# Performance work log

Hardware: AMD Instinct MI355X
Metric: run time of the kernel (lower is better)

## Reference

```python
import jax, jax.numpy as jnp
import numpy as np

B, IN, OUT = 256, 1024, 1024

def leaky_clamp(x, lo, hi, slope):
    return jnp.where(x < lo, lo + slope * (x - lo),
           jnp.where(x > hi, hi + slope * (x - hi), x))

def setup_inputs() -> dict:
    key = jax.random.key(0)
    kx, kw = jax.random.split(key)
    x = jax.random.normal(kx, (B, IN), dtype=jnp.float32)
    # xavier_normal for (out,in): std = sqrt(2/(in+out))
    std = np.sqrt(2.0 / (IN + OUT)).astype(np.float32)
    weight = jax.random.normal(kw, (OUT, IN), dtype=jnp.float32) * std
    log_tau = jnp.zeros((), dtype=jnp.float32)
    return {"x": x, "weight": weight, "log_tau": log_tau}

def reference(x, weight, log_tau):
    # actual_weight = leaky_clamp(weight, 0, 1, 0.1)
    aw = leaky_clamp(weight, 0.0, 1.0, 0.1)          # (OUT, IN)
    tau = jnp.exp(log_tau)                            # scalar
    z = x[:, None, :] * aw[None, :, :]                # (B, OUT, IN)
    p = jax.nn.softmax(tau * z, axis=-1)              # (B, OUT, IN)
    s = jnp.sum(p * z, axis=-1)                       # (B, OUT)
    return s
```

## Files before the change

### kernel.cpp

```cpp
#include <hip/hip_runtime.h>

#define BB   256
#define IN_  1024
#define OUTN 1024

#define TB  16
#define TO  16
#define KC  256
#define NS  (IN_ / KC)
#define PAD 4

#define LOG2E 1.4426950408889634f

typedef float v2f __attribute__((ext_vector_type(2)));
typedef float v4f __attribute__((ext_vector_type(4)));

__device__ __forceinline__ float leaky_clamp01(float v) {
    return __builtin_amdgcn_fmed3f(v, 0.1f * v, fmaf(0.1f, v, 0.9f));
}

__global__ __launch_bounds__(256, 4)
void esm_fused_kernel(const float* __restrict__ x,
                      const float* __restrict__ w,
                      const float* __restrict__ log_tau,
                      float* __restrict__ out) {
    __shared__ float xs[TB][KC + PAD];
    __shared__ float wls[TO][KC + PAD];

    const int tid = threadIdx.x;
    const int bid = blockIdx.x;
    const int bt = bid >> 6;
    const int ot = bid & 63;
    const int b0 = bt * TB;
    const int o0 = ot * TO;

    const float scale = __expf(log_tau[0]) * LOG2E;

    const int h    = tid >> 6;
    const int cell = tid & 63;
    const int tx   = cell & 7;
    const int ty   = cell >> 3;
    const int ih   = h << 2;

    const int srow = tid >> 6;
    const int si4  = (tid & 63) << 2;

    float4 rx[4], rw[4];
    #pragma unroll
    for (int t = 0; t < 4; ++t) {
        const int row = srow + t * 4;
        rx[t] = *(const float4*)&x[(size_t)(b0 + row) * IN_ + si4];
        rw[t] = *(const float4*)&w[(size_t)(o0 + row) * IN_ + si4];
    }

    v2f d00 = {0.f, 0.f}, d01 = {0.f, 0.f}, d10 = {0.f, 0.f}, d11 = {0.f, 0.f};
    v2f n00 = {0.f, 0.f}, n01 = {0.f, 0.f}, n10 = {0.f, 0.f}, n11 = {0.f, 0.f};

    #pragma unroll
    for (int s = 0; s < NS; ++s) {
        if (s) __syncthreads();
        #pragma unroll
        for (int t = 0; t < 4; ++t) {
            const int row = srow + t * 4;
            const float4 xv = rx[t];
            float4 xo;
            xo.x = xv.x * scale; xo.y = xv.y * scale;
            xo.z = xv.z * scale; xo.w = xv.w * scale;
            *(float4*)&xs[row][si4] = xo;
            const float4 wv = rw[t];
            float4 wo;
            wo.x = leaky_clamp01(wv.x); wo.y = leaky_clamp01(wv.y);
            wo.z = leaky_clamp01(wv.z); wo.w = leaky_clamp01(wv.w);
            *(float4*)&wls[row][si4] = wo;
        }
        __syncthreads();
        if (s + 1 < NS) {
            const int i0n = (s + 1) * KC;
            #pragma unroll
            for (int t = 0; t < 4; ++t) {
                const int row = srow + t * 4;
                rx[t] = *(const float4*)&x[(size_t)(b0 + row) * IN_ + i0n + si4];
                rw[t] = *(const float4*)&w[(size_t)(o0 + row) * IN_ + i0n + si4];
            }
        }

        #pragma unroll 4
        for (int m = 0; m < KC / 16; ++m) {
            const int ib = 16 * m + ih;
            const v4f xa0 = *(const v4f*)&xs[2 * ty][ib];
            const v4f xa1 = *(const v4f*)&xs[2 * ty + 1][ib];
            const v4f wa0 = *(const v4f*)&wls[2 * tx][ib];
            const v4f wa1 = *(const v4f*)&wls[2 * tx + 1][ib];
            #pragma unroll
            for (int p = 0; p < 2; ++p) {
                const v2f xv0 = {xa0[2 * p], xa0[2 * p + 1]};
                const v2f xv1 = {xa1[2 * p], xa1[2 * p + 1]};
                const v2f wv0 = {wa0[2 * p], wa0[2 * p + 1]};
                const v2f wv1 = {wa1[2 * p], wa1[2 * p + 1]};
                const v2f t00 = xv0 * wv0;
                const v2f t01 = xv0 * wv1;
                const v2f t10 = xv1 * wv0;
                const v2f t11 = xv1 * wv1;
                v2f e00, e01, e10, e11;
                e00.x = __builtin_amdgcn_exp2f(t00.x);
                e00.y = __builtin_amdgcn_exp2f(t00.y);
                e01.x = __builtin_amdgcn_exp2f(t01.x);
                e01.y = __builtin_amdgcn_exp2f(t01.y);
                e10.x = __builtin_amdgcn_exp2f(t10.x);
                e10.y = __builtin_amdgcn_exp2f(t10.y);
                e11.x = __builtin_amdgcn_exp2f(t11.x);
                e11.y = __builtin_amdgcn_exp2f(t11.y);
                d00 += e00; d01 += e01; d10 += e10; d11 += e11;
                n00 = __builtin_elementwise_fma(e00, t00, n00);
                n01 = __builtin_elementwise_fma(e01, t01, n01);
                n10 = __builtin_elementwise_fma(e10, t10, n10);
                n11 = __builtin_elementwise_fma(e11, t11, n11);
            }
        }
    }

    const float d00s = d00.x + d00.y, n00s = n00.x + n00.y;
    const float d01s = d01.x + d01.y, n01s = n01.x + n01.y;
    const float d10s = d10.x + d10.y, n10s = n10.x + n10.y;
    const float d11s = d11.x + d11.y, n11s = n11.x + n11.y;

    __syncthreads();
    float* sd = &xs[0][0];
    float* sn = &wls[0][0];
    const int co00 = (2 * ty) * 16 + 2 * tx;
    sd[(h << 8) + co00]      = d00s;
    sd[(h << 8) + co00 + 1]  = d01s;
    sd[(h << 8) + co00 + 16] = d10s;
    sd[(h << 8) + co00 + 17] = d11s;
    sn[(h << 8) + co00]      = n00s;
    sn[(h << 8) + co00 + 1]  = n01s;
    sn[(h << 8) + co00 + 16] = n10s;
    sn[(h << 8) + co00 + 17] = n11s;
    __syncthreads();
    if (h == 0) {
        float dt00 = 0.f, dt01 = 0.f, dt10 = 0.f, dt11 = 0.f;
        float nt00 = 0.f, nt01 = 0.f, nt10 = 0.f, nt11 = 0.f;
        #pragma unroll
        for (int hh = 0; hh < 4; ++hh) {
            const int base = (hh << 8) + co00;
            dt00 += sd[base];      dt01 += sd[base + 1];
            dt10 += sd[base + 16]; dt11 += sd[base + 17];
            nt00 += sn[base];      nt01 += sn[base + 1];
            nt10 += sn[base + 16]; nt11 += sn[base + 17];
        }
        const size_t r0o = (size_t)(b0 + 2 * ty) * OUTN + o0 + 2 * tx;
        const size_t r1o = (size_t)(b0 + 2 * ty + 1) * OUTN + o0 + 2 * tx;
        out[r0o]     = nt00 / (dt00 * scale);
        out[r0o + 1] = nt01 / (dt01 * scale);
        out[r1o]     = nt10 / (dt10 * scale);
        out[r1o + 1] = nt11 / (dt11 * scale);
    }
}

extern "C" void kernel_launch(void* const* d_in, const int* in_sizes, int n_in,
                              void* d_out, int out_size, void* d_ws, size_t ws_size,
                              hipStream_t stream) {
    const float* x  = (const float*)d_in[0];
    const float* w  = (const float*)d_in[1];
    const float* lt = (const float*)d_in[2];
    float* out = (float*)d_out;

    esm_fused_kernel<<<(BB / TB) * (OUTN / TO), 256, 0, stream>>>(x, w, lt, out);
}
```

Baseline: 91.29 us.

## Make weight tile resident in LDS and loop over batch tiles per block

Each block now loads and clamps a full 16x1024 weight tile into LDS once, then iterates over four batch tiles, streaming in only the x tile for each and prefetching the next one into registers. Blocks grow to 1024 threads splitting K 16 ways, shared memory is XOR-swizzled, and the grid shrinks to 256 blocks. This removes redundant weight loads and clamps across batch tiles and the per-chunk syncs. The cost is 128 KB of LDS per block, one block per CU, and a 16-way cross-thread reduction through LDS for every batch tile.

```diff
diff --git a/kernel.cpp b/kernel.cpp
--- a/kernel.cpp
+++ b/kernel.cpp
@@ -6,9 +6,7 @@
 
 #define TB  16
 #define TO  16
-#define KC  256
-#define NS  (IN_ / KC)
-#define PAD 4
+#define NR  4
 
 #define LOG2E 1.4426950408889634f
 
@@ -19,20 +17,23 @@
     return __builtin_amdgcn_fmed3f(v, 0.1f * v, fmaf(0.1f, v, 0.9f));
 }
 
-__global__ __launch_bounds__(256, 4)
+__device__ __forceinline__ int swz(int r, int g) {
+    return r * 1024 + ((g ^ (r & 7)) << 2);
+}
+
+__global__ __launch_bounds__(1024, 4)
 void esm_fused_kernel(const float* __restrict__ x,
                       const float* __restrict__ w,
                       const float* __restrict__ log_tau,
                       float* __restrict__ out) {
-    __shared__ float xs[TB][KC + PAD];
-    __shared__ float wls[TO][KC + PAD];
+    __shared__ float xs[TB * 1024];
+    __shared__ float wls[TO * 1024];
 
     const int tid = threadIdx.x;
-    const int bid = blockIdx.x;
-    const int bt = bid >> 6;
-    const int ot = bid & 63;
-    const int b0 = bt * TB;
-    const int o0 = ot * TO;
+    const int p   = blockIdx.x;
+    const int ot  = p & 63;
+    const int btb = p >> 6;
+    const int o0  = ot * TO;
 
     const float scale = __expf(log_tau[0]) * LOG2E;
 
@@ -40,63 +41,63 @@
     const int cell = tid & 63;
     const int tx   = cell & 7;
     const int ty   = cell >> 3;
-    const int ih   = h << 2;
 
-    const int srow = tid >> 6;
-    const int si4  = (tid & 63) << 2;
+    const int srow = tid >> 8;
+    const int scol = tid & 255;
 
     float4 rx[4], rw[4];
     #pragma unroll
     for (int t = 0; t < 4; ++t) {
-        const int row = srow + t * 4;
-        rx[t] = *(const float4*)&x[(size_t)(b0 + row) * IN_ + si4];
-        rw[t] = *(const float4*)&w[(size_t)(o0 + row) * IN_ + si4];
+        const int row = srow + 4 * t;
+        rw[t] = *(const float4*)&w[(size_t)(o0 + row) * IN_ + (scol << 2)];
+        rx[t] = *(const float4*)&x[(size_t)(btb * TB + row) * IN_ + (scol << 2)];
     }
+    #pragma unroll
+    for (int t = 0; t < 4; ++t) {
+        const int row = srow + 4 * t;
+        const float4 wv = rw[t];
+        float4 wo;
+        wo.x = leaky_clamp01(wv.x); wo.y = leaky_clamp01(wv.y);
+        wo.z = leaky_clamp01(wv.z); wo.w = leaky_clamp01(wv.w);
+        *(float4*)&wls[swz(row, scol)] = wo;
+        const float4 xv = rx[t];
+        float4 xo;
+        xo.x = xv.x * scale; xo.y = xv.y * scale;
+        xo.z = xv.z * scale; xo.w = xv.w * scale;
+        *(float4*)&xs[swz(row, scol)] = xo;
+    }
+    __syncthreads();
 
-    v2f d00 = {0.f, 0.f}, d01 = {0.f, 0.f}, d10 = {0.f, 0.f}, d11 = {0.f, 0.f};
-    v2f n00 = {0.f, 0.f}, n01 = {0.f, 0.f}, n10 = {0.f, 0.f}, n11 = {0.f, 0.f};
+    const float* xr0 = &xs[2 * ty * 1024 + ((h ^ ((2 * ty) & 7)) << 2)];
+    const float* xr1 = &xs[(2 * ty + 1) * 1024 + ((h ^ ((2 * ty + 1) & 7)) << 2)];
+    const float* wr0 = &wls[2 * tx * 1024 + ((h ^ ((2 * tx) & 7)) << 2)];
+    const float* wr1 = &wls[(2 * tx + 1) * 1024 + ((h ^ ((2 * tx + 1) & 7)) << 2)];
 
     #pragma unroll
-    for (int s = 0; s < NS; ++s) {
-        if (s) __syncthreads();
-        #pragma unroll
-        for (int t = 0; t < 4; ++t) {
-            const int row = srow + t * 4;
-            const float4 xv = rx[t];
-            float4 xo;
-            xo.x = xv.x * scale; xo.y = xv.y * scale;
-            xo.z = xv.z * scale; xo.w = xv.w * scale;
-            *(float4*)&xs[row][si4] = xo;
-            const float4 wv = rw[t];
-            float4 wo;
-            wo.x = leaky_clamp01(wv.x); wo.y = leaky_clamp01(wv.y);
-            wo.z = leaky_clamp01(wv.z); wo.w = leaky_clamp01(wv.w);
-            *(float4*)&wls[row][si4] = wo;
-        }
-        __syncthreads();
-        if (s + 1 < NS) {
-            const int i0n = (s + 1) * KC;
+    for (int r = 0; r < NR; ++r) {
+        const int b0 = (4 * r + btb) * TB;
+
+        if (r + 1 < NR) {
+            const int b0n = (4 * (r + 1) + btb) * TB;
             #pragma unroll
-            for (int t = 0; t < 4; ++t) {
-                const int row = srow + t * 4;
-                rx[t] = *(const float4*)&x[(size_t)(b0 + row) * IN_ + i0n + si4];
-                rw[t] = *(const float4*)&w[(size_t)(o0 + row) * IN_ + i0n + si4];
-            }
+            for (int t = 0; t < 4; ++t)
+                rx[t] = *(const float4*)&x[(size_t)(b0n + srow + 4 * t) * IN_ + (scol << 2)];
         }
 
+        v2f d00 = {0.f, 0.f}, d01 = {0.f, 0.f}, d10 = {0.f, 0.f}, d11 = {0.f, 0.f};
+        v2f n00 = {0.f, 0.f}, n01 = {0.f, 0.f}, n10 = {0.f, 0.f}, n11 = {0.f, 0.f};
         #pragma unroll 4
-        for (int m = 0; m < KC / 16; ++m) {
-            const int ib = 16 * m + ih;
-            const v4f xa0 = *(const v4f*)&xs[2 * ty][ib];
-            const v4f xa1 = *(const v4f*)&xs[2 * ty + 1][ib];
-            const v4f wa0 = *(const v4f*)&wls[2 * tx][ib];
-            const v4f wa1 = *(const v4f*)&wls[2 * tx + 1][ib];
+        for (int m = 0; m < 16; ++m) {
+            const v4f xa0 = *(const v4f*)(xr0 + (m << 6));
+            const v4f xa1 = *(const v4f*)(xr1 + (m << 6));
+            const v4f wa0 = *(const v4f*)(wr0 + (m << 6));
+            const v4f wa1 = *(const v4f*)(wr1 + (m << 6));
             #pragma unroll
-            for (int p = 0; p < 2; ++p) {
-                const v2f xv0 = {xa0[2 * p], xa0[2 * p + 1]};
-                const v2f xv1 = {xa1[2 * p], xa1[2 * p + 1]};
-                const v2f wv0 = {wa0[2 * p], wa0[2 * p + 1]};
-                const v2f wv1 = {wa1[2 * p], wa1[2 * p + 1]};
+            for (int q = 0; q < 2; ++q) {
+                const v2f xv0 = {xa0[2 * q], xa0[2 * q + 1]};
+                const v2f xv1 = {xa1[2 * q], xa1[2 * q + 1]};
+                const v2f wv0 = {wa0[2 * q], wa0[2 * q + 1]};
+                const v2f wv1 = {wa1[2 * q], wa1[2 * q + 1]};
                 const v2f t00 = xv0 * wv0;
                 const v2f t01 = xv0 * wv1;
                 const v2f t10 = xv1 * wv0;
@@ -117,43 +118,48 @@
                 n11 = __builtin_elementwise_fma(e11, t11, n11);
             }
         }
-    }
 
-    const float d00s = d00.x + d00.y, n00s = n00.x + n00.y;
-    const float d01s = d01.x + d01.y, n01s = n01.x + n01.y;
-    const float d10s = d10.x + d10.y, n10s = n10.x + n10.y;
-    const float d11s = d11.x + d11.y, n11s = n11.x + n11.y;
+        const float d00s = d00.x + d00.y, n00s = n00.x + n00.y;
+        const float d01s = d01.x + d01.y, n01s = n01.x + n01.y;
+        const float d10s = d10.x + d10.y, n10s = n10.x + n10.y;
+        const float d11s = d11.x + d11.y, n11s = n11.x + n11.y;
 
-    __syncthreads();
-    float* sd = &xs[0][0];
-    float* sn = &wls[0][0];
-    const int co00 = (2 * ty) * 16 + 2 * tx;
-    sd[(h << 8) + co00]      = d00s;
-    sd[(h << 8) + co00 + 1]  = d01s;
-    sd[(h << 8) + co00 + 16] = d10s;
-    sd[(h << 8) + co00 + 17] = d11s;
-    sn[(h << 8) + co00]      = n00s;
-    sn[(h << 8) + co00 + 1]  = n01s;
-    sn[(h << 8) + co00 + 16] = n10s;
-    sn[(h << 8) + co00 + 17] = n11s;
-    __syncthreads();
-    if (h == 0) {
-        float dt00 = 0.f, dt01 = 0.f, dt10 = 0.f, dt11 = 0.f;
-        float nt00 = 0.f, nt01 = 0.f, nt10 = 0.f, nt11 = 0.f;
-        #pragma unroll
-        for (int hh = 0; hh < 4; ++hh) {
-            const int base = (hh << 8) + co00;
-            dt00 += sd[base];      dt01 += sd[base + 1];
-            dt10 += sd[base + 16]; dt11 += sd[base + 17];
-            nt00 += sn[base];      nt01 += sn[base + 1];
-            nt10 += sn[base + 16]; nt11 += sn[base + 17];
+        __syncthreads();
+        float* sd = xs;
+        float* sn = xs + 4096;
+        const int co = 32 * ty + 2 * tx;
+        sd[(h << 8) + co]      = d00s;
+        sd[(h << 8) + co + 1]  = d01s;
+        sd[(h << 8) + co + 16] = d10s;
+        sd[(h << 8) + co + 17] = d11s;
+        sn[(h << 8) + co]      = n00s;
+        sn[(h << 8) + co + 1]  = n01s;
+        sn[(h << 8) + co + 16] = n10s;
+        sn[(h << 8) + co + 17] = n11s;
+        __syncthreads();
+        if (tid < 256) {
+            float dt = 0.f, nt = 0.f;
+            #pragma unroll
+            for (int hh = 0; hh < 16; ++hh) {
+                dt += sd[(hh << 8) + tid];
+                nt += sn[(hh << 8) + tid];
+            }
+            out[(size_t)(b0 + (tid >> 4)) * OUTN + o0 + (tid & 15)] = nt / (dt * scale);
         }
-        const size_t r0o = (size_t)(b0 + 2 * ty) * OUTN + o0 + 2 * tx;
-        const size_t r1o = (size_t)(b0 + 2 * ty + 1) * OUTN + o0 + 2 * tx;
-        out[r0o]     = nt00 / (dt00 * scale);
-        out[r0o + 1] = nt01 / (dt01 * scale);
-        out[r1o]     = nt10 / (dt10 * scale);
-        out[r1o + 1] = nt11 / (dt11 * scale);
+
+        if (r + 1 < NR) {
+            __syncthreads();
+            #pragma unroll
+            for (int t = 0; t < 4; ++t) {
+                const int row = srow + 4 * t;
+                const float4 xv = rx[t];
+                float4 xo;
+                xo.x = xv.x * scale; xo.y = xv.y * scale;
+                xo.z = xv.z * scale; xo.w = xv.w * scale;
+                *(float4*)&xs[swz(row, scol)] = xo;
+            }
+            __syncthreads();
+        }
     }
 }
 
@@ -165,5 +171,5 @@
     const float* lt = (const float*)d_in[2];
     float* out = (float*)d_out;
 
-    esm_fused_kernel<<<(BB / TB) * (OUTN / TO), 256, 0, stream>>>(x, w, lt, out);
+    esm_fused_kernel<<<256, 1024, 0, stream>>>(x, w, lt, out);
 }
```

New measurement: 94.14 us. 3.1% more time.
